# Optimization experiments

Hardware: AMD Instinct MI355X
Metric: run time of the kernel (lower is better)

Reference implementation:

```python
import jax, jax.numpy as jnp
import numpy as np

N = 100_000          # nodes
E = 3_200_000        # edges (avg degree 32)
IN, HID, OUT = 128, 64, 40
POWERS = [6, 8, 10]
MAXP = 10
LN_EPS = 1e-5


def setup_inputs() -> dict:
    key = jax.random.key(0)
    ks = jax.random.split(key, 8)
    x = jax.random.normal(ks[0], (N, IN), jnp.float32)
    edge_index = jax.random.randint(ks[1], (2, E), 0, N, dtype=jnp.int32)
    # params (torch Linear: y = x @ W + b with W stored [in, out] here)
    W1 = jax.random.normal(ks[2], (IN, HID), jnp.float32) / np.sqrt(IN)
    b1 = jnp.zeros((HID,), jnp.float32)
    # MixHopConv has Linear for every power 0..max(powers); only p in POWERS are used
    Wc = jax.random.normal(ks[3], (MAXP + 1, HID, HID), jnp.float32) / np.sqrt(HID)
    bc = jnp.zeros((MAXP + 1, HID), jnp.float32)
    W2 = jax.random.normal(ks[4], (HID * len(POWERS), OUT), jnp.float32) / np.sqrt(HID * len(POWERS))
    b2 = jnp.zeros((OUT,), jnp.float32)
    g1 = jnp.ones((HID,), jnp.float32); be1 = jnp.zeros((HID,), jnp.float32)
    g2 = jnp.ones((HID * len(POWERS),), jnp.float32); be2 = jnp.zeros((HID * len(POWERS),), jnp.float32)
    return dict(x=x, edge_index=edge_index, W1=W1, b1=b1, Wc=Wc, bc=bc,
                W2=W2, b2=b2, g1=g1, be1=be1, g2=g2, be2=be2)


def _layer_norm(h, g, b):
    mu = jnp.mean(h, axis=-1, keepdims=True)
    var = jnp.mean(jnp.square(h - mu), axis=-1, keepdims=True)
    return (h - mu) * jax.lax.rsqrt(var + LN_EPS) * g + b


def _gcn_norm(edge_index, n, dtype):
    # add self loops (fill 1), symmetric normalization D^-1/2 (A+I) D^-1/2
    loops = jnp.arange(n, dtype=edge_index.dtype)
    src = jnp.concatenate([edge_index[0], loops])
    dst = jnp.concatenate([edge_index[1], loops])
    w = jnp.ones(src.shape[0], dtype)
    deg = jax.ops.segment_sum(w, dst, num_segments=n)
    dis = jnp.where(deg > 0, jax.lax.rsqrt(deg), 0.0)
    norm = dis[src] * w * dis[dst]
    return src, dst, norm


def reference(x, edge_index, W1, b1, Wc, bc, W2, b2, g1, be1, g2, be2):
    n = x.shape[0]
    src, dst, norm = _gcn_norm(edge_index, n, x.dtype)

    def propagate(h):  # out[i] = sum_{(j->i)} norm_ij * h[j]
        return jax.ops.segment_sum(norm[:, None] * h[src], dst, num_segments=n)

    h = jax.nn.gelu(x @ W1 + b1, approximate=False)
    h = _layer_norm(h, g1, be1)
    # dropout is identity in eval mode

    # MixHop: propagate MAXP times, apply per-power linear at p in POWERS
    outs = {}
    if 0 in POWERS:
        outs[0] = h @ Wc[0] + bc[0]
    cur = h
    for j in range(1, MAXP + 1):
        cur = propagate(cur)
        if j in POWERS:
            outs[j] = cur @ Wc[j] + bc[j]
    h = jnp.concatenate([outs[p] for p in POWERS], axis=-1)

    h = jax.nn.gelu(h, approximate=False)
    h = _layer_norm(h, g2, be2)
    return h @ W2 + b2
```

## Files before the change

kernel.cpp:

```cpp
#include <hip/hip_runtime.h>

typedef _Float16 h16;
typedef _Float16 h16x8 __attribute__((ext_vector_type(8)));
typedef short short8 __attribute__((ext_vector_type(8)));
typedef float f32x4 __attribute__((ext_vector_type(4)));

__device__ __forceinline__ float bf2f(unsigned short u) {
    return __uint_as_float(((unsigned)u) << 16);
}
__device__ __forceinline__ unsigned short f2bf(float f) {
    unsigned x = __float_as_uint(f);
    unsigned r = x + 0x7fffu + ((x >> 16) & 1u);
    return (unsigned short)(r >> 16);
}
__device__ __forceinline__ float gelu_fast(float v) {
    float y = 0.7978845608f * (v + 0.044715f * v * v * v);
    float e = __expf(2.0f * y);
    float th = 1.0f - 2.0f * __builtin_amdgcn_rcpf(e + 1.0f);
    return 0.5f * v * (1.0f + th);
}

__device__ __forceinline__ float ldin(const void* p, size_t i, int isbf) {
    return isbf ? bf2f(((const unsigned short*)p)[i]) : ((const float*)p)[i];
}

#define LN_EPS 1e-5f
#define NBMAX 256
#define NBLK 1024

__global__ void k_flag(const unsigned* __restrict__ g1w, int* __restrict__ flag) {
    if (blockIdx.x == 0 && threadIdx.x == 0)
        *flag = (g1w[0] == 0x3F803F80u) ? 1 : 0;
}

__global__ void k_bcnt(const int* __restrict__ dst, int* __restrict__ bcnt,
                       int* __restrict__ cnts, int E, int chunk) {
    __shared__ int c[NBMAX];
    int t = threadIdx.x, blk = blockIdx.x;
    c[t] = 0;
    __syncthreads();
    int beg = blk * chunk;
    int end = beg + chunk; if (end > E) end = E;
    for (int i = beg + t; i < end; i += 256)
        atomicAdd(&c[dst[i] >> 9], 1);
    __syncthreads();
    cnts[blk * NBMAX + t] = c[t];
    if (c[t] > 0) atomicAdd(&bcnt[t], c[t]);
}

__global__ void k_bscan(const int* __restrict__ bcnt, int* __restrict__ bbase, int NB) {
    __shared__ int sh[NBMAX];
    int t = threadIdx.x;
    int v = (t < NB) ? bcnt[t] : 0;
    sh[t] = v;
    __syncthreads();
    for (int s = 1; s < 256; s <<= 1) {
        int u = 0;
        if (t >= s) u = sh[t - s];
        __syncthreads();
        sh[t] += u;
        __syncthreads();
    }
    if (t < NB) bbase[t] = sh[t] - v;
    if (t == 0) bbase[NB] = sh[NBMAX - 1];
}

__global__ void k_colscan(const int* __restrict__ cnts, const int* __restrict__ bbase,
                          int* __restrict__ base) {
    __shared__ int sh[256];
    int b = blockIdx.x, t = threadIdx.x;
    int v[NBLK / 256];
    int s = 0;
#pragma unroll
    for (int j = 0; j < NBLK / 256; j++) {
        v[j] = cnts[(size_t)(t * (NBLK / 256) + j) * NBMAX + b];
        s += v[j];
    }
    sh[t] = s;
    __syncthreads();
    for (int st = 1; st < 256; st <<= 1) {
        int u = 0;
        if (t >= st) u = sh[t - st];
        __syncthreads();
        sh[t] += u;
        __syncthreads();
    }
    int run = bbase[b] + (t == 0 ? 0 : sh[t - 1]);
#pragma unroll
    for (int j = 0; j < NBLK / 256; j++) {
        base[(size_t)(t * (NBLK / 256) + j) * NBMAX + b] = run;
        run += v[j];
    }
}

__global__ void k_bin(const int* __restrict__ src, const int* __restrict__ dst,
                      const int* __restrict__ base, unsigned* __restrict__ stg,
                      int E, int chunk) {
    __shared__ int loc[NBMAX];
    int t = threadIdx.x, blk = blockIdx.x;
    loc[t] = base[(size_t)blk * NBMAX + t];
    __syncthreads();
    int beg = blk * chunk;
    int end = beg + chunk; if (end > E) end = E;
    for (int i = beg + t; i < end; i += 256) {
        int s = src[i], d = dst[i];
        int b = d >> 9;
        unsigned pr = ((unsigned)(d & 511) << 23) | (unsigned)s;
        int p = atomicAdd(&loc[b], 1);
        stg[p] = pr;
    }
}

__global__ void k_build2(const unsigned* __restrict__ stg, const int* __restrict__ bbase,
                         int* __restrict__ offv, float* __restrict__ dis,
                         float* __restrict__ d2, float* __restrict__ idis,
                         int* __restrict__ csr, int N, int E, int NB) {
    __shared__ int cnt[512];
    __shared__ int sc[512];
    __shared__ int pos[512];
    int b = blockIdx.x, t = threadIdx.x;
    cnt[t] = 0; cnt[t + 256] = 0;
    __syncthreads();
    int beg = bbase[b], end = bbase[b + 1];
    for (int k = beg + t; k < end; k += 256)
        atomicAdd(&cnt[stg[k] >> 23], 1);
    __syncthreads();
    sc[t] = cnt[t]; sc[t + 256] = cnt[t + 256];
    pos[t] = 0; pos[t + 256] = 0;
    __syncthreads();
    for (int s = 1; s < 512; s <<= 1) {
        int u0 = 0, u1 = 0;
        if (t >= s) u0 = sc[t - s];
        if (t + 256 >= s) u1 = sc[t + 256 - s];
        __syncthreads();
        sc[t] += u0; sc[t + 256] += u1;
        __syncthreads();
    }
    int nb9 = b << 9;
#pragma unroll
    for (int ii = 0; ii < 2; ii++) {
        int i = t + ii * 256;
        int node = nb9 + i;
        if (node < N) {
            offv[node] = beg + sc[i] - cnt[i];
            float dp1 = (float)(cnt[i] + 1);
            dis[node] = rsqrtf(dp1);
            d2[node] = 1.0f / dp1;
            idis[node] = sqrtf(dp1);
        }
    }
    if (b == NB - 1 && t == 0) offv[N] = E;
    __syncthreads();
    for (int k = beg + t; k < end; k += 256) {
        unsigned pr = stg[k];
        int dl = (int)(pr >> 23);
        int p = beg + (sc[dl] - cnt[dl]) + atomicAdd(&pos[dl], 1);
        csr[p] = (int)(pr & 0x7FFFFFu);
    }
}

__global__ void k_in(const void* __restrict__ x, const void* __restrict__ W1,
                     const void* __restrict__ b1, const void* __restrict__ g1,
                     const void* __restrict__ be1, const float* __restrict__ dis,
                     h16* __restrict__ h, const int* __restrict__ flag, int N) {
    __shared__ __align__(16) short Bf[4][4][64][8];
    int isbf = *flag;
    int tid = threadIdx.x;
    for (int idx = tid; idx < 4 * 4 * 64; idx += 256) {
        int c = idx >> 8, t = (idx >> 6) & 3, ln = idx & 63;
        int quad = ln >> 4, col = t * 16 + (ln & 15);
#pragma unroll
        for (int j = 0; j < 8; j++) {
            int k = c * 32 + quad * 8 + j;
            Bf[c][t][ln][j] = (short)f2bf(ldin(W1, (size_t)k * 64 + col, isbf));
        }
    }
    __syncthreads();
    int lane = tid & 63, quad = lane >> 4, m15 = lane & 15;
    float bcol[4], gcol[4], ecol[4];
#pragma unroll
    for (int t = 0; t < 4; t++) {
        int col = t * 16 + m15;
        bcol[t] = ldin(b1, col, isbf);
        gcol[t] = ldin(g1, col, isbf);
        ecol[t] = ldin(be1, col, isbf);
    }
    int wave = blockIdx.x * 4 + (tid >> 6);
    int nwave = gridDim.x * 4;
    int ntile = (N + 15) >> 4;
    for (int tile = wave; tile < ntile; tile += nwave) {
        int m0 = tile << 4;
        int mrow = m0 + m15; if (mrow >= N) mrow = N - 1;
        f32x4 acc[4];
#pragma unroll
        for (int t = 0; t < 4; t++)
#pragma unroll
            for (int r = 0; r < 4; r++) acc[t][r] = 0.0f;
#pragma unroll
        for (int c = 0; c < 4; c++) {
            short8 a;
            if (isbf) {
                a = *(const short8*)((const unsigned short*)x + (size_t)mrow * 128 + c * 32 + quad * 8);
            } else {
                const float* xp = (const float*)x + (size_t)mrow * 128 + c * 32 + quad * 8;
#pragma unroll
                for (int j = 0; j < 8; j++) a[j] = (short)f2bf(xp[j]);
            }
#pragma unroll
            for (int t = 0; t < 4; t++) {
                short8 b = *(const short8*)(&Bf[c][t][lane][0]);
                acc[t] = __builtin_amdgcn_mfma_f32_16x16x32_bf16(a, b, acc[t], 0, 0, 0);
            }
        }
        float v[4][4];
        float s[4] = {0, 0, 0, 0}, q[4] = {0, 0, 0, 0};
#pragma unroll
        for (int t = 0; t < 4; t++)
#pragma unroll
            for (int r = 0; r < 4; r++) {
                float g = gelu_fast(acc[t][r] + bcol[t]);
                v[t][r] = g;
                s[r] += g; q[r] += g * g;
            }
#pragma unroll
        for (int o = 1; o < 16; o <<= 1)
#pragma unroll
            for (int r = 0; r < 4; r++) {
                s[r] += __shfl_xor(s[r], o, 64);
                q[r] += __shfl_xor(q[r], o, 64);
            }
#pragma unroll
        for (int r = 0; r < 4; r++) {
            int node = m0 + quad * 4 + r;
            if (node < N) {
                float mu = s[r] * (1.0f / 64.0f);
                float var = q[r] * (1.0f / 64.0f) - mu * mu;
                float rs = rsqrtf(var + LN_EPS);
                float dn = dis[node];
#pragma unroll
                for (int t = 0; t < 4; t++) {
                    float hv = (v[t][r] - mu) * rs * gcol[t] + ecol[t];
                    h[(size_t)node * 64 + t * 16 + m15] = (h16)(dn * hv);
                }
            }
        }
    }
}

__global__ void k_prop(const h16* __restrict__ cur, h16* __restrict__ nxt,
                       const int* __restrict__ offv, const int* __restrict__ csr,
                       const float* __restrict__ d2, int N) {
    int node = blockIdx.x * 4 + (threadIdx.x >> 6);
    if (node >= N) return;
    int lane = threadIdx.x & 63;
    int g = lane >> 3, q = lane & 7;
    h16x8 acc = {0, 0, 0, 0, 0, 0, 0, 0};
    int e = offv[node], end = offv[node + 1];
#pragma unroll 2
    for (; e + 8 <= end; e += 8) {
        int s = csr[e + g];
        acc += *(const h16x8*)(cur + (size_t)s * 64 + q * 8);
    }
    int r = end - e;
    if (g < r) {
        int s = csr[e + g];
        acc += *(const h16x8*)(cur + (size_t)s * 64 + q * 8);
    }
#pragma unroll
    for (int o = 8; o < 64; o <<= 1) {
        h16x8 other;
        int* ap = (int*)&acc;
        int* op = (int*)&other;
#pragma unroll
        for (int i = 0; i < 4; i++) op[i] = __shfl_xor(ap[i], o, 64);
        acc += other;
    }
    if (g == 0) {
        float dd = d2[node];
        h16x8 sv = *(const h16x8*)(cur + (size_t)node * 64 + q * 8);
        h16x8 o8;
#pragma unroll
        for (int i = 0; i < 8; i++) o8[i] = (h16)(dd * ((float)acc[i] + (float)sv[i]));
        *(h16x8*)(nxt + (size_t)node * 64 + q * 8) = o8;
    }
}

__global__ void k_pout(const h16* __restrict__ cur, const void* __restrict__ Wc,
                       const void* __restrict__ bc, const float* __restrict__ idis,
                       h16* __restrict__ hcat, const int* __restrict__ flag,
                       size_t woff, size_t boff, int seg, int N) {
    __shared__ __align__(16) h16 Bf[2][4][64][8];
    int isbf = *flag;
    int tid = threadIdx.x;
    for (int idx = tid; idx < 2 * 4 * 64; idx += 256) {
        int c = idx >> 8, t = (idx >> 6) & 3, ln = idx & 63;
        int quad = ln >> 4, col = t * 16 + (ln & 15);
#pragma unroll
        for (int j = 0; j < 8; j++) {
            int k = c * 32 + quad * 8 + j;
            Bf[c][t][ln][j] = (h16)ldin(Wc, woff + (size_t)k * 64 + col, isbf);
        }
    }
    __syncthreads();
    int lane = tid & 63, quad = lane >> 4, m15 = lane & 15;
    float bcol[4];
#pragma unroll
    for (int t = 0; t < 4; t++) bcol[t] = ldin(bc, boff + t * 16 + m15, isbf);
    int wave = blockIdx.x * 4 + (tid >> 6);
    int nwave = gridDim.x * 4;
    int ntile = (N + 15) >> 4;
    for (int tile = wave; tile < ntile; tile += nwave) {
        int m0 = tile << 4;
        int mrow = m0 + m15; if (mrow >= N) mrow = N - 1;
        f32x4 acc[4];
#pragma unroll
        for (int t = 0; t < 4; t++)
#pragma unroll
            for (int r = 0; r < 4; r++) acc[t][r] = 0.0f;
#pragma unroll
        for (int c = 0; c < 2; c++) {
            h16x8 a = *(const h16x8*)(cur + (size_t)mrow * 64 + c * 32 + quad * 8);
#pragma unroll
            for (int t = 0; t < 4; t++) {
                h16x8 b = *(const h16x8*)(&Bf[c][t][lane][0]);
                acc[t] = __builtin_amdgcn_mfma_f32_16x16x32_f16(a, b, acc[t], 0, 0, 0);
            }
        }
#pragma unroll
        for (int r = 0; r < 4; r++) {
            int node = m0 + quad * 4 + r;
            if (node < N) {
                float di = idis[node];
#pragma unroll
                for (int t = 0; t < 4; t++)
                    hcat[(size_t)node * 192 + seg * 64 + t * 16 + m15] =
                        (h16)(bcol[t] + di * acc[t][r]);
            }
        }
    }
}

__global__ void k_fin(const h16* __restrict__ hcat, const void* __restrict__ g2,
                      const void* __restrict__ be2, const void* __restrict__ W2,
                      const void* __restrict__ b2, void* __restrict__ out,
                      const int* __restrict__ flag, int N) {
    __shared__ __align__(16) h16 Bf[6][3][64][8];
    __shared__ float2 GB[192];
    __shared__ __align__(16) h16 Y[4][16][200];
    int isbf = *flag;
    int tid = threadIdx.x;
    for (int idx = tid; idx < 6 * 3 * 64; idx += 256) {
        int c = idx / 192, rem = idx % 192;
        int t = rem >> 6, ln = rem & 63;
        int quad = ln >> 4, col = t * 16 + (ln & 15);
#pragma unroll
        for (int j = 0; j < 8; j++) {
            int k = c * 32 + quad * 8 + j;
            float w = (col < 40) ? ldin(W2, (size_t)k * 40 + col, isbf) : 0.0f;
            Bf[c][t][ln][j] = (h16)w;
        }
    }
    for (int i = tid; i < 192; i += 256) {
        float2 gb; gb.x = ldin(g2, i, isbf); gb.y = ldin(be2, i, isbf);
        GB[i] = gb;
    }
    __syncthreads();
    int wv = tid >> 6;
    int lane = tid & 63, quad = lane >> 4, m15 = lane & 15;
    float b2v[3];
#pragma unroll
    for (int t = 0; t < 3; t++) {
        int col = t * 16 + m15;
        b2v[t] = (col < 40) ? ldin(b2, col, isbf) : 0.0f;
    }
    int wave = blockIdx.x * 4 + wv;
    int nwave = gridDim.x * 4;
    int ntile = (N + 15) >> 4;
    for (int tile = wave; tile < ntile; tile += nwave) {
        int m0 = tile << 4;
        int mrow = m0 + m15; if (mrow >= N) mrow = N - 1;
        const h16* hp = hcat + (size_t)mrow * 192 + quad * 48;
        float s = 0.0f, q = 0.0f;
#pragma unroll
        for (int u = 0; u < 6; u++) {
            h16x8 vv = *(const h16x8*)(hp + u * 8);
            h16x8 gv;
#pragma unroll
            for (int j = 0; j < 8; j++) {
                float g = gelu_fast((float)vv[j]);
                gv[j] = (h16)g;
                s += g; q += g * g;
            }
            *(h16x8*)(&Y[wv][m15][quad * 48 + u * 8]) = gv;
        }
        s += __shfl_xor(s, 16, 64); s += __shfl_xor(s, 32, 64);
        q += __shfl_xor(q, 16, 64); q += __shfl_xor(q, 32, 64);
        float mu = s * (1.0f / 192.0f);
        float var = q * (1.0f / 192.0f) - mu * mu;
        float rs = rsqrtf(var + LN_EPS);
        asm volatile("s_waitcnt lgkmcnt(0)" ::: "memory");
        f32x4 acc[3];
#pragma unroll
        for (int t = 0; t < 3; t++)
#pragma unroll
            for (int r = 0; r < 4; r++) acc[t][r] = 0.0f;
#pragma unroll
        for (int c = 0; c < 6; c++) {
            h16x8 raw = *(const h16x8*)(&Y[wv][m15][c * 32 + quad * 8]);
            h16x8 a;
#pragma unroll
            for (int j = 0; j < 8; j++) {
                int k = c * 32 + quad * 8 + j;
                float2 gb = GB[k];
                a[j] = (h16)(((float)raw[j] - mu) * rs * gb.x + gb.y);
            }
#pragma unroll
            for (int t = 0; t < 3; t++) {
                h16x8 b = *(const h16x8*)(&Bf[c][t][lane][0]);
                acc[t] = __builtin_amdgcn_mfma_f32_16x16x32_f16(a, b, acc[t], 0, 0, 0);
            }
        }
        asm volatile("" ::: "memory");
#pragma unroll
        for (int r = 0; r < 4; r++) {
            int node = m0 + quad * 4 + r;
            if (node < N) {
#pragma unroll
                for (int t = 0; t < 3; t++) {
                    int col = t * 16 + m15;
                    if (col < 40) {
                        float o = acc[t][r] + b2v[t];
                        if (isbf) ((unsigned short*)out)[(size_t)node * 40 + col] = f2bf(o);
                        else      ((float*)out)[(size_t)node * 40 + col] = o;
                    }
                }
            }
        }
    }
}

extern "C" void kernel_launch(void* const* d_in, const int* in_sizes, int n_in,
                              void* d_out, int out_size, void* d_ws, size_t ws_size,
                              hipStream_t stream) {
    const int IN = 128, HID = 64;
    const int N = in_sizes[0] / IN;
    const int E = in_sizes[1] / 2;
    const int NB = (N + 511) >> 9;
    const int chunk = (E + NBLK - 1) / NBLK;

    const void* x   = d_in[0];
    const int*  ei  = (const int*)d_in[1];
    const void* W1  = d_in[2];
    const void* b1  = d_in[3];
    const void* Wc  = d_in[4];
    const void* bc  = d_in[5];
    const void* W2  = d_in[6];
    const void* b2  = d_in[7];
    const void* g1  = d_in[8];
    const void* be1 = d_in[9];
    const void* g2  = d_in[10];
    const void* be2 = d_in[11];

    char* ws = (char*)d_ws;
    size_t off = 0;
    auto take = [&](size_t bytes) -> char* {
        char* p = ws + off;
        off = (off + bytes + 255) & ~(size_t)255;
        return p;
    };
    int*   flag  = (int*)take(256);
    int*   bcnt  = (int*)take(NBMAX * 4);
    int*   bbase = (int*)take((NBMAX + 1) * 4);
    float* dis   = (float*)take((size_t)N * 4);
    float* d2    = (float*)take((size_t)N * 4);
    float* idis  = (float*)take((size_t)N * 4);
    int*   offv  = (int*)take((size_t)(N + 1) * 4);
    int*   csr   = (int*)take((size_t)E * 4);
    size_t unionSz = (size_t)E * 4 > (size_t)N * 384 ? (size_t)E * 4 : (size_t)N * 384;
    char*  uni   = take(unionSz);
    unsigned* stg = (unsigned*)uni;
    h16*   hcat  = (h16*)uni;
    h16*   hA    = (h16*)take((size_t)N * HID * 2);
    h16*   hB    = (h16*)take((size_t)N * HID * 2);
    int*   cnts  = csr;
    int*   base  = csr + (size_t)NBLK * NBMAX;

    hipMemsetAsync(bcnt, 0, NBMAX * 4, stream);

    const int* srcp = ei;
    const int* dstp = ei + E;
    int gNode = (N + 3) / 4;
    int gDense = 1563;

    k_flag<<<1, 64, 0, stream>>>((const unsigned*)g1, flag);
    k_bcnt<<<NBLK, 256, 0, stream>>>(dstp, bcnt, cnts, E, chunk);
    k_bscan<<<1, 256, 0, stream>>>(bcnt, bbase, NB);
    k_colscan<<<NB, 256, 0, stream>>>(cnts, bbase, base);
    k_bin<<<NBLK, 256, 0, stream>>>(srcp, dstp, base, stg, E, chunk);
    k_build2<<<NB, 256, 0, stream>>>(stg, bbase, offv, dis, d2, idis, csr, N, E, NB);

    k_in<<<gDense, 256, 0, stream>>>(x, W1, b1, g1, be1, dis, hA, flag, N);
    h16* cur = hA; h16* nxt = hB;
    int seg = 0;
    for (int j = 1; j <= 10; j++) {
        k_prop<<<gNode, 256, 0, stream>>>(cur, nxt, offv, csr, d2, N);
        h16* tmp = cur; cur = nxt; nxt = tmp;
        if (j == 6 || j == 8 || j == 10) {
            k_pout<<<gDense, 256, 0, stream>>>(cur, Wc, bc, idis, hcat, flag,
                                               (size_t)j * HID * HID, (size_t)j * HID,
                                               seg, N);
            seg++;
        }
    }
    k_fin<<<gDense, 256, 0, stream>>>(hcat, g2, be2, W2, b2, d_out, flag, N);
}
```

Baseline: 910.2 us.

## Split features into two 32-wide planes and propagate each plane separately

The 64-wide hidden state is stored as two 32-column fp16 planes, and the ten propagation steps run over one plane and then over the other. Each plane (about 6.4 MB) is more likely to stay in the on-chip L2/LLC during random neighbour gathers. The gather kernel now handles 16 edges per iteration with 4 lanes per row. Weight conversion and layout is moved into a one-time prep kernel so the dense kernels only copy pre-swizzled weights, and the final kernel keeps GELU outputs in registers instead of staging them in LDS. In exchange the number of propagation launches doubles and each gather moves only 64 bytes per neighbour.

Measured after the change: 1.280 ms. 1.41x slower.

```diff
diff --git a/kernel.cpp b/kernel.cpp
--- a/kernel.cpp
+++ b/kernel.cpp
@@ -31,6 +31,70 @@
 __global__ void k_flag(const unsigned* __restrict__ g1w, int* __restrict__ flag) {
     if (blockIdx.x == 0 && threadIdx.x == 0)
         *flag = (g1w[0] == 0x3F803F80u) ? 1 : 0;
+}
+
+__global__ void k_prep(const void* __restrict__ W1, const void* __restrict__ b1,
+                       const void* __restrict__ g1, const void* __restrict__ be1,
+                       const void* __restrict__ Wc, const void* __restrict__ bc,
+                       const void* __restrict__ W2, const void* __restrict__ b2,
+                       const void* __restrict__ g2, const void* __restrict__ be2,
+                       const int* __restrict__ flag,
+                       short* __restrict__ W1f, h16* __restrict__ Wcf,
+                       h16* __restrict__ W2f, float* __restrict__ vecs,
+                       float2* __restrict__ GBv) {
+    int isbf = *flag;
+    int t = threadIdx.x, b = blockIdx.x;
+    if (b == 0) {
+        for (int idx = t; idx < 1024; idx += 256) {
+            int c = idx >> 8, tt = (idx >> 6) & 3, ln = idx & 63;
+            int quad = ln >> 4, col = tt * 16 + (ln & 15);
+#pragma unroll
+            for (int j = 0; j < 8; j++) {
+                int k = c * 32 + quad * 8 + j;
+                W1f[idx * 8 + j] = (short)f2bf(ldin(W1, (size_t)k * 64 + col, isbf));
+            }
+        }
+    } else if (b <= 3) {
+        int s = b - 1;
+        int js = (s == 0) ? 6 : (s == 1) ? 8 : 10;
+        size_t woff = (size_t)js * 64 * 64;
+        h16* Wp = Wcf + (size_t)s * 4096;
+        for (int idx = t; idx < 512; idx += 256) {
+            int c = idx >> 8, tt = (idx >> 6) & 3, ln = idx & 63;
+            int quad = ln >> 4, col = tt * 16 + (ln & 15);
+#pragma unroll
+            for (int j = 0; j < 8; j++) {
+                int k = c * 32 + quad * 8 + j;
+                Wp[idx * 8 + j] = (h16)ldin(Wc, woff + (size_t)k * 64 + col, isbf);
+            }
+        }
+    } else if (b == 4) {
+        for (int idx = t; idx < 1152; idx += 256) {
+            int c = idx / 192, rem = idx % 192;
+            int tt = rem >> 6, ln = rem & 63;
+            int quad = ln >> 4, col = tt * 16 + (ln & 15);
+#pragma unroll
+            for (int j = 0; j < 8; j++) {
+                int k = c * 32 + quad * 8 + j;
+                float w = (col < 40) ? ldin(W2, (size_t)k * 40 + col, isbf) : 0.0f;
+                W2f[idx * 8 + j] = (h16)w;
+            }
+        }
+    } else {
+        if (t < 64) {
+            vecs[t]       = ldin(b1, t, isbf);
+            vecs[64 + t]  = ldin(g1, t, isbf);
+            vecs[128 + t] = ldin(be1, t, isbf);
+            vecs[192 + t] = ldin(bc, (size_t)6 * 64 + t, isbf);
+            vecs[256 + t] = ldin(bc, (size_t)8 * 64 + t, isbf);
+            vecs[320 + t] = ldin(bc, (size_t)10 * 64 + t, isbf);
+        }
+        if (t < 40) vecs[384 + t] = ldin(b2, t, isbf);
+        if (t < 192) {
+            float2 gb; gb.x = ldin(g2, t, isbf); gb.y = ldin(be2, t, isbf);
+            GBv[t] = gb;
+        }
+    }
 }
 
 __global__ void k_bcnt(const int* __restrict__ dst, int* __restrict__ bcnt,
@@ -159,21 +223,17 @@
     }
 }
 
-__global__ void k_in(const void* __restrict__ x, const void* __restrict__ W1,
-                     const void* __restrict__ b1, const void* __restrict__ g1,
-                     const void* __restrict__ be1, const float* __restrict__ dis,
-                     h16* __restrict__ h, const int* __restrict__ flag, int N) {
+__global__ void k_in(const void* __restrict__ x, const short* __restrict__ W1f,
+                     const float* __restrict__ vecs, const float* __restrict__ dis,
+                     h16* __restrict__ o0, h16* __restrict__ o1,
+                     const int* __restrict__ flag, int N) {
     __shared__ __align__(16) short Bf[4][4][64][8];
     int isbf = *flag;
     int tid = threadIdx.x;
-    for (int idx = tid; idx < 4 * 4 * 64; idx += 256) {
-        int c = idx >> 8, t = (idx >> 6) & 3, ln = idx & 63;
-        int quad = ln >> 4, col = t * 16 + (ln & 15);
-#pragma unroll
-        for (int j = 0; j < 8; j++) {
-            int k = c * 32 + quad * 8 + j;
-            Bf[c][t][ln][j] = (short)f2bf(ldin(W1, (size_t)k * 64 + col, isbf));
-        }
+    {
+        int4* d = (int4*)&Bf[0][0][0][0];
+        const int4* s4 = (const int4*)W1f;
+        for (int i = tid; i < 1024; i += 256) d[i] = s4[i];
     }
     __syncthreads();
     int lane = tid & 63, quad = lane >> 4, m15 = lane & 15;
@@ -181,9 +241,9 @@
 #pragma unroll
     for (int t = 0; t < 4; t++) {
         int col = t * 16 + m15;
-        bcol[t] = ldin(b1, col, isbf);
-        gcol[t] = ldin(g1, col, isbf);
-        ecol[t] = ldin(be1, col, isbf);
+        bcol[t] = vecs[col];
+        gcol[t] = vecs[64 + col];
+        ecol[t] = vecs[128 + col];
     }
     int wave = blockIdx.x * 4 + (tid >> 6);
     int nwave = gridDim.x * 4;
@@ -240,7 +300,8 @@
 #pragma unroll
                 for (int t = 0; t < 4; t++) {
                     float hv = (v[t][r] - mu) * rs * gcol[t] + ecol[t];
-                    h[(size_t)node * 64 + t * 16 + m15] = (h16)(dn * hv);
+                    h16* op = (t < 2) ? o0 : o1;
+                    op[(size_t)node * 32 + (t & 1) * 16 + m15] = (h16)(dn * hv);
                 }
             }
         }
@@ -253,21 +314,21 @@
     int node = blockIdx.x * 4 + (threadIdx.x >> 6);
     if (node >= N) return;
     int lane = threadIdx.x & 63;
-    int g = lane >> 3, q = lane & 7;
+    int g = lane >> 2, q = lane & 3;
     h16x8 acc = {0, 0, 0, 0, 0, 0, 0, 0};
     int e = offv[node], end = offv[node + 1];
 #pragma unroll 2
-    for (; e + 8 <= end; e += 8) {
+    for (; e + 16 <= end; e += 16) {
         int s = csr[e + g];
-        acc += *(const h16x8*)(cur + (size_t)s * 64 + q * 8);
+        acc += *(const h16x8*)(cur + (size_t)s * 32 + q * 8);
     }
     int r = end - e;
     if (g < r) {
         int s = csr[e + g];
-        acc += *(const h16x8*)(cur + (size_t)s * 64 + q * 8);
-    }
-#pragma unroll
-    for (int o = 8; o < 64; o <<= 1) {
+        acc += *(const h16x8*)(cur + (size_t)s * 32 + q * 8);
+    }
+#pragma unroll
+    for (int o = 4; o < 64; o <<= 1) {
         h16x8 other;
         int* ap = (int*)&acc;
         int* op = (int*)&other;
@@ -277,35 +338,29 @@
     }
     if (g == 0) {
         float dd = d2[node];
-        h16x8 sv = *(const h16x8*)(cur + (size_t)node * 64 + q * 8);
+        h16x8 sv = *(const h16x8*)(cur + (size_t)node * 32 + q * 8);
         h16x8 o8;
 #pragma unroll
         for (int i = 0; i < 8; i++) o8[i] = (h16)(dd * ((float)acc[i] + (float)sv[i]));
-        *(h16x8*)(nxt + (size_t)node * 64 + q * 8) = o8;
-    }
-}
-
-__global__ void k_pout(const h16* __restrict__ cur, const void* __restrict__ Wc,
-                       const void* __restrict__ bc, const float* __restrict__ idis,
-                       h16* __restrict__ hcat, const int* __restrict__ flag,
-                       size_t woff, size_t boff, int seg, int N) {
+        *(h16x8*)(nxt + (size_t)node * 32 + q * 8) = o8;
+    }
+}
+
+__global__ void k_pout(h16* __restrict__ p0, h16* __restrict__ p1,
+                       const h16* __restrict__ Wcf, const float* __restrict__ bcv,
+                       const float* __restrict__ idis, int N) {
     __shared__ __align__(16) h16 Bf[2][4][64][8];
-    int isbf = *flag;
     int tid = threadIdx.x;
-    for (int idx = tid; idx < 2 * 4 * 64; idx += 256) {
-        int c = idx >> 8, t = (idx >> 6) & 3, ln = idx & 63;
-        int quad = ln >> 4, col = t * 16 + (ln & 15);
-#pragma unroll
-        for (int j = 0; j < 8; j++) {
-            int k = c * 32 + quad * 8 + j;
-            Bf[c][t][ln][j] = (h16)ldin(Wc, woff + (size_t)k * 64 + col, isbf);
-        }
+    {
+        int4* d = (int4*)&Bf[0][0][0][0];
+        const int4* s4 = (const int4*)Wcf;
+        for (int i = tid; i < 512; i += 256) d[i] = s4[i];
     }
     __syncthreads();
     int lane = tid & 63, quad = lane >> 4, m15 = lane & 15;
     float bcol[4];
 #pragma unroll
-    for (int t = 0; t < 4; t++) bcol[t] = ldin(bc, boff + t * 16 + m15, isbf);
+    for (int t = 0; t < 4; t++) bcol[t] = bcv[t * 16 + m15];
     int wave = blockIdx.x * 4 + (tid >> 6);
     int nwave = gridDim.x * 4;
     int ntile = (N + 15) >> 4;
@@ -319,7 +374,8 @@
             for (int r = 0; r < 4; r++) acc[t][r] = 0.0f;
 #pragma unroll
         for (int c = 0; c < 2; c++) {
-            h16x8 a = *(const h16x8*)(cur + (size_t)mrow * 64 + c * 32 + quad * 8);
+            const h16* ip = c ? p1 : p0;
+            h16x8 a = *(const h16x8*)(ip + (size_t)mrow * 32 + quad * 8);
 #pragma unroll
             for (int t = 0; t < 4; t++) {
                 h16x8 b = *(const h16x8*)(&Bf[c][t][lane][0]);
@@ -332,73 +388,65 @@
             if (node < N) {
                 float di = idis[node];
 #pragma unroll
-                for (int t = 0; t < 4; t++)
-                    hcat[(size_t)node * 192 + seg * 64 + t * 16 + m15] =
-                        (h16)(bcol[t] + di * acc[t][r]);
-            }
-        }
-    }
-}
-
-__global__ void k_fin(const h16* __restrict__ hcat, const void* __restrict__ g2,
-                      const void* __restrict__ be2, const void* __restrict__ W2,
-                      const void* __restrict__ b2, void* __restrict__ out,
+                for (int t = 0; t < 4; t++) {
+                    h16 val = (h16)(bcol[t] + di * acc[t][r]);
+                    h16* op = (t < 2) ? p0 : p1;
+                    op[(size_t)node * 32 + (t & 1) * 16 + m15] = val;
+                }
+            }
+        }
+    }
+}
+
+__global__ void k_fin(const h16* __restrict__ P0, const h16* __restrict__ P1,
+                      const h16* __restrict__ P2, const h16* __restrict__ P3,
+                      const h16* __restrict__ P4, const h16* __restrict__ P5,
+                      const h16* __restrict__ W2f, const float* __restrict__ b2v,
+                      const float2* __restrict__ GBv, void* __restrict__ out,
                       const int* __restrict__ flag, int N) {
     __shared__ __align__(16) h16 Bf[6][3][64][8];
-    __shared__ float2 GB[192];
-    __shared__ __align__(16) h16 Y[4][16][200];
+    __shared__ float2 GBs[192];
     int isbf = *flag;
     int tid = threadIdx.x;
-    for (int idx = tid; idx < 6 * 3 * 64; idx += 256) {
-        int c = idx / 192, rem = idx % 192;
-        int t = rem >> 6, ln = rem & 63;
-        int quad = ln >> 4, col = t * 16 + (ln & 15);
-#pragma unroll
-        for (int j = 0; j < 8; j++) {
-            int k = c * 32 + quad * 8 + j;
-            float w = (col < 40) ? ldin(W2, (size_t)k * 40 + col, isbf) : 0.0f;
-            Bf[c][t][ln][j] = (h16)w;
-        }
-    }
-    for (int i = tid; i < 192; i += 256) {
-        float2 gb; gb.x = ldin(g2, i, isbf); gb.y = ldin(be2, i, isbf);
-        GB[i] = gb;
-    }
-    __syncthreads();
-    int wv = tid >> 6;
+    {
+        int4* d = (int4*)&Bf[0][0][0][0];
+        const int4* s4 = (const int4*)W2f;
+        for (int i = tid; i < 1152; i += 256) d[i] = s4[i];
+    }
+    for (int i = tid; i < 192; i += 256) GBs[i] = GBv[i];
+    __syncthreads();
     int lane = tid & 63, quad = lane >> 4, m15 = lane & 15;
-    float b2v[3];
+    float b2c[3];
 #pragma unroll
     for (int t = 0; t < 3; t++) {
         int col = t * 16 + m15;
-        b2v[t] = (col < 40) ? ldin(b2, col, isbf) : 0.0f;
-    }
-    int wave = blockIdx.x * 4 + wv;
+        b2c[t] = (col < 40) ? b2v[col] : 0.0f;
+    }
+    int wave = blockIdx.x * 4 + (tid >> 6);
     int nwave = gridDim.x * 4;
     int ntile = (N + 15) >> 4;
     for (int tile = wave; tile < ntile; tile += nwave) {
         int m0 = tile << 4;
         int mrow = m0 + m15; if (mrow >= N) mrow = N - 1;
-        const h16* hp = hcat + (size_t)mrow * 192 + quad * 48;
+        h16x8 v6[6];
         float s = 0.0f, q = 0.0f;
 #pragma unroll
         for (int u = 0; u < 6; u++) {
-            h16x8 vv = *(const h16x8*)(hp + u * 8);
-            h16x8 gv;
+            const h16* Pu = (u == 0) ? P0 : (u == 1) ? P1 : (u == 2) ? P2
+                          : (u == 3) ? P3 : (u == 4) ? P4 : P5;
+            h16x8 vv = *(const h16x8*)(Pu + (size_t)mrow * 32 + quad * 8);
 #pragma unroll
             for (int j = 0; j < 8; j++) {
                 float g = gelu_fast((float)vv[j]);
-                gv[j] = (h16)g;
+                v6[u][j] = (h16)g;
                 s += g; q += g * g;
             }
-            *(h16x8*)(&Y[wv][m15][quad * 48 + u * 8]) = gv;
         }
         s += __shfl_xor(s, 16, 64); s += __shfl_xor(s, 32, 64);
         q += __shfl_xor(q, 16, 64); q += __shfl_xor(q, 32, 64);
         float mu = s * (1.0f / 192.0f);
         float var = q * (1.0f / 192.0f) - mu * mu;
         float rs = rsqrtf(var + LN_EPS);
-        asm volatile("s_waitcnt lgkmcnt(0)" ::: "memory");
         f32x4 acc[3];
 #pragma unroll
         for (int t = 0; t < 3; t++)
@@ -406,13 +454,11 @@
             for (int r = 0; r < 4; r++) acc[t][r] = 0.0f;
 #pragma unroll
         for (int c = 0; c < 6; c++) {
-            h16x8 raw = *(const h16x8*)(&Y[wv][m15][c * 32 + quad * 8]);
             h16x8 a;
 #pragma unroll
             for (int j = 0; j < 8; j++) {
-                int k = c * 32 + quad * 8 + j;
-                float2 gb = GB[k];
-                a[j] = (h16)(((float)raw[j] - mu) * rs * gb.x + gb.y);
+                float2 gb = GBs[c * 32 + quad * 8 + j];
+                a[j] = (h16)(((float)v6[c][j] - mu) * rs * gb.x + gb.y);
             }
 #pragma unroll
             for (int t = 0; t < 3; t++) {
@@ -420,7 +466,6 @@
                 acc[t] = __builtin_amdgcn_mfma_f32_16x16x32_f16(a, b, acc[t], 0, 0, 0);
             }
         }
-        asm volatile("" ::: "memory");
 #pragma unroll
         for (int r = 0; r < 4; r++) {
             int node = m0 + quad * 4 + r;
@@ -429,7 +474,7 @@
                 for (int t = 0; t < 3; t++) {
                     int col = t * 16 + m15;
                     if (col < 40) {
-                        float o = acc[t][r] + b2v[t];
+                        float o = acc[t][r] + b2c[t];
                         if (isbf) ((unsigned short*)out)[(size_t)node * 40 + col] = f2bf(o);
                         else      ((float*)out)[(size_t)node * 40 + col] = o;
                     }
@@ -442,7 +487,7 @@
 extern "C" void kernel_launch(void* const* d_in, const int* in_sizes, int n_in,
                               void* d_out, int out_size, void* d_ws, size_t ws_size,
                               hipStream_t stream) {
-    const int IN = 128, HID = 64;
+    const int IN = 128;
     const int N = in_sizes[0] / IN;
     const int E = in_sizes[1] / 2;
     const int NB = (N + 511) >> 9;
@@ -476,12 +521,22 @@
     float* idis  = (float*)take((size_t)N * 4);
     int*   offv  = (int*)take((size_t)(N + 1) * 4);
     int*   csr   = (int*)take((size_t)E * 4);
-    size_t unionSz = (size_t)E * 4 > (size_t)N * 384 ? (size_t)E * 4 : (size_t)N * 384;
+    size_t planeB  = (size_t)N * 32 * 2;
+    size_t unionSz = (size_t)E * 4 > 2 * planeB ? (size_t)E * 4 : 2 * planeB;
     char*  uni   = take(unionSz);
     unsigned* stg = (unsigned*)uni;
-    h16*   hcat  = (h16*)uni;
-    h16*   hA    = (h16*)take((size_t)N * HID * 2);
-    h16*   hB    = (h16*)take((size_t)N * HID * 2);
+    h16*   I0    = (h16*)uni;
+    h16*   I1    = (h16*)(uni + planeB);
+    h16*   Bsh   = (h16*)take(planeB);
+    h16*   SC[2][3];
+    for (int p = 0; p < 2; p++)
+        for (int s = 0; s < 3; s++)
+            SC[p][s] = (h16*)take(planeB);
+    short* W1f  = (short*)take(16384);
+    h16*   Wcf  = (h16*)take(24576);
+    h16*   W2f  = (h16*)take(18432);
+    float* vecs = (float*)take(2048);
+    float2* GBv = (float2*)take(1536);
     int*   cnts  = csr;
     int*   base  = csr + (size_t)NBLK * NBMAX;
 
@@ -493,24 +548,30 @@
     int gDense = 1563;
 
     k_flag<<<1, 64, 0, stream>>>((const unsigned*)g1, flag);
+    k_prep<<<6, 256, 0, stream>>>(W1, b1, g1, be1, Wc, bc, W2, b2, g2, be2, flag,
+                                  W1f, Wcf, W2f, vecs, GBv);
     k_bcnt<<<NBLK, 256, 0, stream>>>(dstp, bcnt, cnts, E, chunk);
     k_bscan<<<1, 256, 0, stream>>>(bcnt, bbase, NB);
     k_colscan<<<NB, 256, 0, stream>>>(cnts, bbase, base);
     k_bin<<<NBLK, 256, 0, stream>>>(srcp, dstp, base, stg, E, chunk);
     k_build2<<<NB, 256, 0, stream>>>(stg, bbase, offv, dis, d2, idis, csr, N, E, NB);
 
-    k_in<<<gDense, 256, 0, stream>>>(x, W1, b1, g1, be1, dis, hA, flag, N);
-    h16* cur = hA; h16* nxt = hB;
-    int seg = 0;
-    for (int j = 1; j <= 10; j++) {
-        k_prop<<<gNode, 256, 0, stream>>>(cur, nxt, offv, csr, d2, N);
-        h16* tmp = cur; cur = nxt; nxt = tmp;
-        if (j == 6 || j == 8 || j == 10) {
-            k_pout<<<gDense, 256, 0, stream>>>(cur, Wc, bc, idis, hcat, flag,
-                                               (size_t)j * HID * HID, (size_t)j * HID,
-                                               seg, N);
-            seg++;
-        }
-    }
-    k_fin<<<gDense, 256, 0, stream>>>(hcat, g2, be2, W2, b2, d_out, flag, N);
-}
+    k_in<<<gDense, 256, 0, stream>>>(x, W1f, vecs, dis, I0, I1, flag, N);
+
+    for (int p = 0; p < 2; p++) {
+        h16* A = p ? I1 : I0;
+        h16* s6 = SC[p][0]; h16* s8 = SC[p][1]; h16* s10 = SC[p][2];
+        h16* seq[10][2] = {
+            {A, Bsh}, {Bsh, A}, {A, Bsh}, {Bsh, A}, {A, Bsh},
+            {Bsh, s6}, {s6, A}, {A, s8}, {s8, Bsh}, {Bsh, s10}};
+        for (int j = 0; j < 10; j++)
+            k_prop<<<gNode, 256, 0, stream>>>(seq[j][0], seq[j][1], offv, csr, d2, N);
+    }
+    for (int s = 0; s < 3; s++)
+        k_pout<<<gDense, 256, 0, stream>>>(SC[0][s], SC[1][s],
+                                           Wcf + (size_t)s * 4096,
+                                           vecs + 192 + s * 64, idis, N);
+    k_fin<<<gDense, 256, 0, stream>>>(SC[0][0], SC[1][0], SC[0][1], SC[1][1],
+                                      SC[0][2], SC[1][2],
+                                      W2f, vecs + 384, GBv, d_out, flag, N);
+}
```
